# Kernel tuning notes

Hardware: AMD Instinct MI355X
Metric: run time of the kernel (lower is better)

The kernel has to match this reference:

```python
import jax, jax.numpy as jnp
import numpy as np

B = 65536


def conv1d(x, w, b=None, stride=1, pad=0):
    # x: [B, C_in, L], w: [C_out, C_in, K]
    y = jax.lax.conv_general_dilated(x, w, (stride,), [(pad, pad)],
                                     dimension_numbers=('NCH', 'OIH', 'NCH'))
    if b is not None:
        y = y + b[None, :, None]
    return y


def setup_inputs() -> dict:
    key = jax.random.key(0)
    ks = jax.random.split(key, 17)
    s = 0.05
    return {
        'data': jax.random.normal(ks[0], (B, 512), jnp.float32),
        'sr': 16000,
        'stft_w': jax.random.normal(ks[1], (258, 1, 256), jnp.float32) * s,
        'e1_w': jax.random.normal(ks[2], (128, 129, 3), jnp.float32) * s,
        'e1_b': jax.random.normal(ks[3], (128,), jnp.float32) * s,
        'e2_w': jax.random.normal(ks[4], (64, 128, 3), jnp.float32) * s,
        'e2_b': jax.random.normal(ks[5], (64,), jnp.float32) * s,
        'e3_w': jax.random.normal(ks[6], (64, 64, 3), jnp.float32) * s,
        'e3_b': jax.random.normal(ks[7], (64,), jnp.float32) * s,
        'e4_w': jax.random.normal(ks[8], (128, 64, 3), jnp.float32) * s,
        'e4_b': jax.random.normal(ks[9], (128,), jnp.float32) * s,
        'w_ih': jax.random.normal(ks[10], (512, 128), jnp.float32) * s,
        'w_hh': jax.random.normal(ks[11], (512, 128), jnp.float32) * s,
        'b_ih': jax.random.normal(ks[12], (512,), jnp.float32) * s,
        'b_hh': jax.random.normal(ks[13], (512,), jnp.float32) * s,
        'dec_w': jax.random.normal(ks[14], (1, 128, 1), jnp.float32) * s,
        'dec_b': jax.random.normal(ks[15], (1,), jnp.float32) * s,
    }


def reference(data, sr, stft_w, e1_w, e1_b, e2_w, e2_b, e3_w, e3_b,
              e4_w, e4_b, w_ih, w_hh, b_ih, b_hh, dec_w, dec_b):
    # First streaming call: zero context, zero LSTM state.
    context_size = 64 if sr == 16000 else 32
    b = data.shape[0]
    ctx = jnp.zeros((b, context_size), data.dtype)
    x = jnp.concatenate([ctx, data], axis=1)          # [B, 576]
    # --- STFT: reflect-pad right by 64, strided conv ---
    x = jnp.pad(x, ((0, 0), (0, 64)), mode='reflect')[:, None, :]  # [B,1,640]
    spec = conv1d(x, stft_w, None, stride=128)         # [B,258,4]
    real = spec[:, :129, :6]
    imag = spec[:, 129:, :6]
    mag = jnp.sqrt(real * real + imag * imag)          # [B,129,4]
    # --- encoder: 4 conv1d + relu blocks ---
    x = jax.nn.relu(conv1d(mag, e1_w, e1_b, 1, 1))     # [B,128,4]
    x = jax.nn.relu(conv1d(x, e2_w, e2_b, 2, 1))       # [B,64,2]
    x = jax.nn.relu(conv1d(x, e3_w, e3_b, 2, 1))       # [B,64,1]
    x = jax.nn.relu(conv1d(x, e4_w, e4_b, 1, 1))       # [B,128,1]
    # --- decoder: LSTMCell (zero initial state) ---
    xt = x[:, :, 0]                                    # squeeze(-1): [B,128]
    h0 = jnp.zeros((b, 128), xt.dtype)
    c0 = jnp.zeros((b, 128), xt.dtype)
    gates = xt @ w_ih.T + b_ih + h0 @ w_hh.T + b_hh    # [B,512]
    i, f, g, o = jnp.split(gates, 4, axis=1)           # torch gate order i,f,g,o
    c = jax.nn.sigmoid(f) * c0 + jax.nn.sigmoid(i) * jnp.tanh(g)
    h = jax.nn.sigmoid(o) * jnp.tanh(c)
    # Dropout is identity in eval mode; then relu, 1x1 conv, sigmoid.
    y = jax.nn.relu(h)[:, :, None]                     # [B,128,1]
    y = jax.nn.sigmoid(conv1d(y, dec_w, dec_b, 1, 0))  # [B,1,1]
    return y
```

## Files before the change

### kernel.cpp

```cpp
#include <hip/hip_runtime.h>


typedef unsigned short u16;
typedef unsigned int u32;
typedef __attribute__((ext_vector_type(8))) short bf16x8;
typedef __attribute__((ext_vector_type(4))) float f32x4;

__device__ __forceinline__ float bf2f(u16 u) {
    return __uint_as_float(((u32)u) << 16);
}
__device__ __forceinline__ u16 f2bf(float f) {
    u32 x = __float_as_uint(f);
    return (u16)((x + 0x7fffu + ((x >> 16) & 1u)) >> 16);
}
__device__ __forceinline__ float sigm(float x) {
    return 1.0f / (1.0f + __expf(-x));
}
__device__ __forceinline__ float tanh_f(float x) {
    float e = __expf(2.0f * x);
    return 1.0f - 2.0f / (e + 1.0f);
}
__device__ __forceinline__ float ldany(const void* p, int idx, int fp32) {
    if (fp32) return ((const float*)p)[idx];
    return bf2f(((const u16*)p)[idx]);
}
__device__ __forceinline__ bf16x8 as_h(uint4 v) {
    union { uint4 u; bf16x8 h; } x; x.u = v; return x.h;
}
#define MFMA(A_, B_, C_) __builtin_amdgcn_mfma_f32_16x16x32_bf16((A_), (B_), (C_), 0, 0, 0)

#define O_WST  0
#define O_W1   34816
#define O_W2   61440
#define O_W3   74752
#define O_W4   78848
#define O_WIH  82944
#define O_B1   115712
#define O_B2   115840
#define O_B3   115904
#define O_B4   115968
#define O_BIH  116096
#define O_DECW 116608
#define O_DECB 116736
#define O_FLAG 116737
#define NCVT   116737

__global__ __launch_bounds__(256) void vad_detect(const void* __restrict__ stft,
                                                  float* __restrict__ dst) {
    if (threadIdx.x == 0 && blockIdx.x == 0) {
        const u16* p = (const u16*)stft;
        int huge = 0;
        for (int i = 0; i < 32; i++) {
            float v = bf2f(p[i]);
            if (!(v == v) || fabsf(v) > 1.0e4f) huge = 1;
        }
        dst[O_FLAG] = huge ? 1.0f : 0.0f;
    }
}

__global__ __launch_bounds__(256) void SileroVAD_83829171683562_kernel(
    void* __restrict__ out, int n, const float* __restrict__ flagp) {
    int i = blockIdx.x * 256 + threadIdx.x;
    int fp32 = (flagp[O_FLAG] != 0.0f);
    if (i < n) {
        if (fp32) ((float*)out)[i] = 0.25f;
        else      ((u16*)out)[i]   = 0x3E80;
    }
}

__device__ __forceinline__ u16 wq_stft(const void* s, int fp32, int j, int k) {
    if (j >= 258) return 0;
    int o = (j >> 1) + (j & 1) * 129;
    return f2bf(ldany(s, o * 256 + k, fp32));
}
__device__ __forceinline__ u16 wq_e1(const void* s, int fp32, int j, int k) {
    if (k >= 408) return 0;
    int tap = k / 136, f = k - tap * 136;
    if (f >= 129) return 0;
    return f2bf(ldany(s, (j * 129 + f) * 3 + tap, fp32));
}
__device__ __forceinline__ u16 wq_e2(const void* s, int fp32, int j, int k) {
    if (k >= 408) return 0;
    int tap = k / 136, c = k - tap * 136;
    if (c >= 128) return 0;
    return f2bf(ldany(s, (j * 128 + c) * 3 + tap, fp32));
}

__global__ __launch_bounds__(256) void vad_cvt_w(
    const void* __restrict__ stft, const void* __restrict__ e1w,
    const void* __restrict__ e1b,  const void* __restrict__ e2w,
    const void* __restrict__ e2b,  const void* __restrict__ e3w,
    const void* __restrict__ e3b,  const void* __restrict__ e4w,
    const void* __restrict__ e4b,  const void* __restrict__ wih,
    const void* __restrict__ bih,  const void* __restrict__ bhh,
    const void* __restrict__ decw, const void* __restrict__ decb,
    float* __restrict__ dst)
{
    int i = blockIdx.x * 256 + threadIdx.x;
    if (i >= NCVT) return;
    int fp32 = (dst[O_FLAG] != 0.0f);
    u32* D = (u32*)dst;
    if (i < O_W1) {
        int t = i * 2, j = t >> 8, k = t & 255;
        D[i] = (u32)wq_stft(stft, fp32, j, k) | ((u32)wq_stft(stft, fp32, j, k + 1) << 16);
    } else if (i < O_W2) {
        int t = (i - O_W1) * 2, j = t / 416, k = t - j * 416;
        D[i] = (u32)wq_e1(e1w, fp32, j, k) | ((u32)wq_e1(e1w, fp32, j, k + 1) << 16);
    } else if (i < O_W3) {
        int t = (i - O_W2) * 2, j = t / 416, k = t - j * 416;
        D[i] = (u32)wq_e2(e2w, fp32, j, k) | ((u32)wq_e2(e2w, fp32, j, k + 1) << 16);
    } else if (i < O_W4) {
        int t = (i - O_W3) * 2, j = t >> 7, c0 = (t & 127) >> 1;
        u16 lo = f2bf(ldany(e3w, (j * 64 + c0) * 3 + 1, fp32));
        u16 hi = f2bf(ldany(e3w, (j * 64 + c0) * 3 + 2, fp32));
        D[i] = (u32)lo | ((u32)hi << 16);
    } else if (i < O_WIH) {
        int t = (i - O_W4) * 2, j = t >> 6, k = t & 63;
        u16 lo = f2bf(ldany(e4w, (j * 64 + k) * 3 + 1, fp32));
        u16 hi = f2bf(ldany(e4w, (j * 64 + k + 1) * 3 + 1, fp32));
        D[i] = (u32)lo | ((u32)hi << 16);
    } else if (i < O_B1) {
        int t = (i - O_WIH) * 2;
        u16 lo = f2bf(ldany(wih, t, fp32));
        u16 hi = f2bf(ldany(wih, t + 1, fp32));
        D[i] = (u32)lo | ((u32)hi << 16);
    } else if (i < O_B2)  dst[i] = ldany(e1b, i - O_B1, fp32);
    else if (i < O_B3)    dst[i] = ldany(e2b, i - O_B2, fp32);
    else if (i < O_B4)    dst[i] = ldany(e3b, i - O_B3, fp32);
    else if (i < O_BIH)   dst[i] = ldany(e4b, i - O_B4, fp32);
    else if (i < O_DECW) { int j = i - O_BIH; dst[i] = ldany(bih, j, fp32) + ldany(bhh, j, fp32); }
    else if (i < O_DECB)  dst[i] = ldany(decw, i - O_DECW, fp32);
    else                  dst[i] = ldany(decb, 0, fp32);
}

__device__ __forceinline__ uint4 load_x8(const void* data, int fp32, int e, int p0) {
    uint4 v;
    if (p0 < 64) { v.x = v.y = v.z = v.w = 0u; return v; }
    if (p0 < 576) {
        if (!fp32)
            return *(const uint4*)((const u16*)data + (size_t)e * 512u + (unsigned)(p0 - 64));
        const float* s = (const float*)data + (size_t)e * 512u + (unsigned)(p0 - 64);
        v.x = (u32)f2bf(s[0]) | ((u32)f2bf(s[1]) << 16);
        v.y = (u32)f2bf(s[2]) | ((u32)f2bf(s[3]) << 16);
        v.z = (u32)f2bf(s[4]) | ((u32)f2bf(s[5]) << 16);
        v.w = (u32)f2bf(s[6]) | ((u32)f2bf(s[7]) << 16);
        return v;
    }
    u16 t[8];
    #pragma unroll
    for (int b = 0; b < 8; b++) {
        int d = 1086 - (p0 + b);
        t[b] = fp32 ? f2bf(((const float*)data)[(size_t)e * 512u + d])
                    : ((const u16*)data)[(size_t)e * 512u + d];
    }
    v.x = (u32)t[0] | ((u32)t[1] << 16);
    v.y = (u32)t[2] | ((u32)t[3] << 16);
    v.z = (u32)t[4] | ((u32)t[5] << 16);
    v.w = (u32)t[6] | ((u32)t[7] << 16);
    return v;
}

#define EB 16
__global__ __launch_bounds__(512, 6) void vad_fused(const void* __restrict__ data,
                                                    const float* __restrict__ W,
                                                    void* __restrict__ out)
{
    __shared__ __align__(16) char smem[48400];
    u16*   XH    = (u16*)smem;
    u16*   OUT1  = (u16*)smem;
    u16*   MAGE1 = (u16*)(smem + 22272);
    u16*   OUT2  = (u16*)(smem + 22272);
    u16*   OUT3  = (u16*)(smem + 30592);
    u16*   OUT4  = (u16*)(smem + 32896);
    float* REDU  = (float*)(smem + 37248);

    const int tid  = threadIdx.x;
    const int w    = __builtin_amdgcn_readfirstlane(tid >> 6);
    const int l    = tid & 63;
    const int l15  = l & 15;
    const int lg   = l >> 4;
    const int b0   = blockIdx.x * EB;
    const int fp32 = (W[O_FLAG] != 0.0f);

    for (int tau = tid; tau < 1280; tau += 512) {
        int ridx = tau >> 4, c8 = tau & 15;
        int e = ridx / 5, h = ridx - e * 5;
        uint4 v = load_x8(data, fp32, b0 + e, h * 128 + c8 * 8);
        *(uint4*)(XH + e * 680 + h * 136 + c8 * 8) = v;
    }
    for (int i = tid; i < 2176; i += 512) {
        int e = i / 136, k = i - e * 136;
        int off = (k < 68) ? k : (k - 68 + 340);
        ((u32*)(MAGE1 + e * 816))[off] = 0u;
    }
    for (int i = tid; i < 448; i += 512) {
        int e = i / 28, r = i - e * 28;
        MAGE1[e * 816 + (r / 7 + 1) * 136 + 129 + (r % 7)] = 0;
    }
    if (tid < 8) MAGE1[16 * 816 + tid] = 0;
    __syncthreads();

    {
        const u16* WB = (const u16*)(W + O_WST);
        const u16* xb0 = XH + (l15 >> 2) * 680 + (l15 & 3) * 136 + lg * 8;
        #pragma unroll 1
        for (int q = 0; q < 3; q++) {
            if (q == 2 && w != 7) break;
            int nt = (q < 2) ? (w * 2 + q) : 16;
            const u16* bp = WB + (nt * 16 + l15) * 256 + lg * 8;
            f32x4 a0 = {0.f,0.f,0.f,0.f}, a1 = {0.f,0.f,0.f,0.f};
            f32x4 a2 = {0.f,0.f,0.f,0.f}, a3 = {0.f,0.f,0.f,0.f};
            uint4 b_0 = *(const uint4*)(bp);
            uint4 b_1 = *(const uint4*)(bp + 32);
            uint4 b_2 = *(const uint4*)(bp + 64);
            uint4 b_3 = *(const uint4*)(bp + 96);
            #pragma unroll 1
            for (int kk = 0; kk < 8; kk++) {
                int kn = (kk < 4) ? (kk + 4) : 7;
                uint4 bn = *(const uint4*)(bp + kn * 32);
                int ao = (kk >> 2) * 136 + (kk & 3) * 32;
                bf16x8 bh = as_h(b_0);
                a0 = MFMA(as_h(*(const uint4*)(xb0 + ao)),        bh, a0);
                a1 = MFMA(as_h(*(const uint4*)(xb0 + 2720 + ao)), bh, a1);
                a2 = MFMA(as_h(*(const uint4*)(xb0 + 5440 + ao)), bh, a2);
                a3 = MFMA(as_h(*(const uint4*)(xb0 + 8160 + ao)), bh, a3);
                b_0 = b_1; b_1 = b_2; b_2 = b_3; b_3 = bn;
            }
            int f = nt * 8 + (l15 >> 1);
            bool wr = ((l15 & 1) == 0) && (f <= 128);
#define ST1_EPI(MT, ACC) do { \
            _Pragma("unroll") \
            for (int r = 0; r < 4; r++) { \
                float v_ = ACC[r]; \
                float p_ = __shfl_xor(v_, 1); \
                float m_ = sqrtf(v_ * v_ + p_ * p_); \
                if (wr) MAGE1[((MT) * 4 + lg) * 816 + (r + 1) * 136 + f] = f2bf(m_); \
            } \
        } while (0)
            ST1_EPI(0, a0); ST1_EPI(1, a1); ST1_EPI(2, a2); ST1_EPI(3, a3);
        }
    }
    __syncthreads();

    for (int i = tid; i < 1472; i += 512) {
        int e = i / 92, k = i - e * 92;
        u32* bz = (u32*)(OUT1 + e * 696);
        int off;
        if (k < 68)      off = k;
        else if (k < 84) { int z = k - 68; off = (z / 4 + 1) * 68 + 64 + (z & 3); }
        else             off = 340 + (k - 84);
        bz[off] = 0u;
    }

    {
        const u16* WB = (const u16*)(W + O_W1);
        const u16* ar0 = MAGE1 + (l15 >> 2) * 816 + (l15 & 3) * 136 + lg * 8;
        int j = w * 16 + l15;
        const u16* bp = WB + j * 416 + lg * 8;
        float bias = W[O_B1 + j];
        f32x4 a0 = {0.f,0.f,0.f,0.f}, a1 = {0.f,0.f,0.f,0.f};
        f32x4 a2 = {0.f,0.f,0.f,0.f}, a3 = {0.f,0.f,0.f,0.f};
        uint4 b_0 = *(const uint4*)(bp);
        uint4 b_1 = *(const uint4*)(bp + 32);
        uint4 b_2 = *(const uint4*)(bp + 64);
        uint4 b_3 = *(const uint4*)(bp + 96);
        #pragma unroll 1
        for (int kk = 0; kk < 13; kk++) {
            int kn = (kk < 9) ? (kk + 4) : 12;
            uint4 bn = *(const uint4*)(bp + kn * 32);
            int ao = kk * 32;
            bf16x8 bh = as_h(b_0);
            a0 = MFMA(as_h(*(const uint4*)(ar0 + ao)),        bh, a0);
            a1 = MFMA(as_h(*(const uint4*)(ar0 + 3264 + ao)), bh, a1);
            a2 = MFMA(as_h(*(const uint4*)(ar0 + 6528 + ao)), bh, a2);
            a3 = MFMA(as_h(*(const uint4*)(ar0 + 9792 + ao)), bh, a3);
            b_0 = b_1; b_1 = b_2; b_2 = b_3; b_3 = bn;
        }
#define ST2_EPI(MT, ACC) do { \
        _Pragma("unroll") \
        for (int r = 0; r < 4; r++) { \
            float v_ = ACC[r] + bias; \
            OUT1[((MT) * 4 + lg) * 696 + (r + 1) * 136 + j] = f2bf(v_ > 0.f ? v_ : 0.f); \
        } \
    } while (0)
        ST2_EPI(0, a0); ST2_EPI(1, a1); ST2_EPI(2, a2); ST2_EPI(3, a3);
    }
    __syncthreads();

    {
        const u16* WB = (const u16*)(W + O_W2);
        int jt = w >> 1, mh = w & 1;
        int j = jt * 16 + l15;
        const u16* bp = WB + j * 416 + lg * 8;
        float bias = W[O_B2 + j];
        const u16* ar0 = OUT1 + (l15 >> 1) * 696 + (l15 & 1) * 272 + lg * 8
                              + mh * 5568;
        f32x4 a0 = {0.f,0.f,0.f,0.f};
        uint4 b_0 = *(const uint4*)(bp);
        uint4 b_1 = *(const uint4*)(bp + 32);
        uint4 b_2 = *(const uint4*)(bp + 64);
        uint4 b_3 = *(const uint4*)(bp + 96);
        #pragma unroll 1
        for (int kk = 0; kk < 13; kk++) {
            int kn = (kk < 9) ? (kk + 4) : 12;
            uint4 bn = *(const uint4*)(bp + kn * 32);
            bf16x8 bh = as_h(b_0);
            a0 = MFMA(as_h(*(const uint4*)(ar0 + kk * 32)), bh, a0);
            b_0 = b_1; b_1 = b_2; b_2 = b_3; b_3 = bn;
        }
        #pragma unroll
        for (int r = 0; r < 4; r++) {
            int rg = mh * 16 + lg * 4 + r;
            float v_ = a0[r] + bias;
            OUT2[(rg >> 1) * 260 + 2 * j + (rg & 1)] = f2bf(v_ > 0.f ? v_ : 0.f);
        }
    }
    __syncthreads();

    if (w < 4) {
        const u16* ap = OUT2 + l15 * 260 + lg * 8;
        const u16* WB = (const u16*)(W + O_W3);
        int j = w * 16 + l15;
        const u16* bp = WB + j * 128 + lg * 8;
        f32x4 acc = {0.f, 0.f, 0.f, 0.f};
        #pragma unroll 1
        for (int kk = 0; kk < 4; kk++)
            acc = MFMA(as_h(*(const uint4*)(ap + kk * 32)),
                       as_h(*(const uint4*)(bp + kk * 32)), acc);
        float bias = W[O_B3 + j];
        #pragma unroll
        for (int r = 0; r < 4; r++) {
            float v = acc[r] + bias;
            OUT3[(lg * 4 + r) * 72 + j] = f2bf(v > 0.f ? v : 0.f);
        }
    }
    __syncthreads();

    {
        const u16* ap = OUT3 + l15 * 72 + lg * 8;
        uint4 a0 = *(const uint4*)(ap);
        uint4 a1 = *(const uint4*)(ap + 32);
        const u16* WB = (const u16*)(W + O_W4);
        int j = w * 16 + l15;
        const u16* bp = WB + j * 64 + lg * 8;
        f32x4 acc = {0.f, 0.f, 0.f, 0.f};
        acc = MFMA(as_h(a0), as_h(*(const uint4*)(bp)), acc);
        acc = MFMA(as_h(a1), as_h(*(const uint4*)(bp + 32)), acc);
        float bias = W[O_B4 + j];
        #pragma unroll
        for (int r = 0; r < 4; r++) {
            float v = acc[r] + bias;
            OUT4[(lg * 4 + r) * 136 + j] = f2bf(v > 0.f ? v : 0.f);
        }
    }
    __syncthreads();

    {
        const u16* ap = OUT4 + l15 * 136 + lg * 8;
        const u16* WB = (const u16*)(W + O_WIH);
        int c = w * 16 + l15;
        const u16* bi = WB + c * 128 + lg * 8;
        f32x4 gi = {0.f,0.f,0.f,0.f}, gg = {0.f,0.f,0.f,0.f}, go = {0.f,0.f,0.f,0.f};
        uint4 Bi = *(const uint4*)(bi);
        uint4 Bg = *(const uint4*)(bi + 32768);
        uint4 Bo = *(const uint4*)(bi + 49152);
        #pragma unroll 1
        for (int kk = 0; kk < 4; kk++) {
            int kn = (kk < 3) ? (kk + 1) : 3;
            uint4 Ni = *(const uint4*)(bi + kn * 32);
            uint4 Ng = *(const uint4*)(bi + 32768 + kn * 32);
            uint4 No = *(const uint4*)(bi + 49152 + kn * 32);
            bf16x8 av = as_h(*(const uint4*)(ap + kk * 32));
            gi = MFMA(av, as_h(Bi), gi);
            gg = MFMA(av, as_h(Bg), gg);
            go = MFMA(av, as_h(Bo), go);
            Bi = Ni; Bg = Ng; Bo = No;
        }
        float bI = W[O_BIH + c], bG = W[O_BIH + 256 + c], bO = W[O_BIH + 384 + c];
        float dw = W[O_DECW + c];
        float part[4];
        #pragma unroll
        for (int r = 0; r < 4; r++) {
            float cs = sigm(gi[r] + bI) * tanh_f(gg[r] + bG);
            float h  = sigm(go[r] + bO) * tanh_f(cs);
            h = h > 0.f ? h : 0.f;
            part[r] = dw * h;
        }
        #pragma unroll
        for (int mk = 1; mk < 16; mk <<= 1) {
            #pragma unroll
            for (int r = 0; r < 4; r++) part[r] += __shfl_xor(part[r], mk);
        }
        if (l15 == 0) {
            #pragma unroll
            for (int r = 0; r < 4; r++) REDU[w * 16 + lg * 4 + r] = part[r];
        }
    }
    __syncthreads();

    if (tid < 16) {
        float s = 0.f;
        #pragma unroll
        for (int ww = 0; ww < 8; ww++) s += REDU[ww * 16 + tid];
        float y = sigm(s + W[O_DECB]);
        if (fp32) ((float*)out)[b0 + tid] = y;
        else      ((u16*)out)[b0 + tid]   = f2bf(y);
    }
}

extern "C" void kernel_launch(void* const* d_in, const int* in_sizes, int n_in,
                              void* d_out, int out_size, void* d_ws, size_t ws_size,
                              hipStream_t stream) {
    (void)in_sizes; (void)n_in; (void)ws_size;
    float* Wf = (float*)d_ws;

    vad_detect<<<1, 64, 0, stream>>>(d_in[2], Wf);

    SileroVAD_83829171683562_kernel<<<(out_size + 255) / 256, 256, 0, stream>>>(
        d_out, out_size, Wf);

    vad_cvt_w<<<(NCVT + 255) / 256, 256, 0, stream>>>(
        d_in[2],  d_in[3],  d_in[4],  d_in[5],  d_in[6],  d_in[7],
        d_in[8],  d_in[9],  d_in[10], d_in[11], d_in[13], d_in[14],
        d_in[15], d_in[16], Wf);

    vad_fused<<<65536 / EB, 512, 0, stream>>>(d_in[0], Wf, d_out);
}
```

Baseline: 448.8 us.

## Fold dtype detection into weight conversion and tighten MFMA loop epilogues

Removes the standalone dtype-detect kernel by having every block of the weight-conversion kernel recompute the flag with a wave vote, saving one launch. In the fused kernel it shortens the B-operand prefetch depth from 4 to 2 and unrolls the MFMA loops. It also swaps sqrtf for raw v_sqrt_f32 and per-element rounding for packed v_cvt_pk_bf16_f32 in the epilogues. The shallower prefetch lowers register pressure but may expose more global-load latency, and the fast sqrt differs slightly in precision.

```diff
diff --git a/kernel.cpp b/kernel.cpp
--- a/kernel.cpp
+++ b/kernel.cpp
@@ -12,6 +12,13 @@
 __device__ __forceinline__ u16 f2bf(float f) {
     u32 x = __float_as_uint(f);
     return (u16)((x + 0x7fffu + ((x >> 16) & 1u)) >> 16);
+}
+__device__ __forceinline__ float sqrt_fast(float x) {
+    float r; asm("v_sqrt_f32 %0, %1" : "=v"(r) : "v"(x)); return r;
+}
+__device__ __forceinline__ u32 cvtpk_bf16(float lo, float hi) {
+    u32 r; asm("v_cvt_pk_bf16_f32 %0, %1, %2" : "=v"(r) : "v"(lo), "v"(hi));
+    return r;
 }
 __device__ __forceinline__ float sigm(float x) {
     return 1.0f / (1.0f + __expf(-x));
@@ -45,19 +52,6 @@
 #define O_FLAG 116737
 #define NCVT   116737
 
-__global__ __launch_bounds__(256) void vad_detect(const void* __restrict__ stft,
-                                                  float* __restrict__ dst) {
-    if (threadIdx.x == 0 && blockIdx.x == 0) {
-        const u16* p = (const u16*)stft;
-        int huge = 0;
-        for (int i = 0; i < 32; i++) {
-            float v = bf2f(p[i]);
-            if (!(v == v) || fabsf(v) > 1.0e4f) huge = 1;
-        }
-        dst[O_FLAG] = huge ? 1.0f : 0.0f;
-    }
-}
-
 __global__ __launch_bounds__(256) void SileroVAD_83829171683562_kernel(
     void* __restrict__ out, int n, const float* __restrict__ flagp) {
     int i = blockIdx.x * 256 + threadIdx.x;
@@ -96,9 +90,23 @@
     const void* __restrict__ decw, const void* __restrict__ decb,
     float* __restrict__ dst)
 {
+    __shared__ int sflag;
+    {
+        int huge = 0;
+        if (threadIdx.x < 64) {
+            if (threadIdx.x < 32) {
+                float v = bf2f(((const u16*)stft)[threadIdx.x]);
+                if (!(v == v) || fabsf(v) > 1.0e4f) huge = 1;
+            }
+            huge = __any(huge);
+            if (threadIdx.x == 0) sflag = huge;
+        }
+        __syncthreads();
+    }
+    int fp32 = sflag;
     int i = blockIdx.x * 256 + threadIdx.x;
+    if (blockIdx.x == 0 && threadIdx.x == 0) dst[O_FLAG] = fp32 ? 1.0f : 0.0f;
     if (i >= NCVT) return;
-    int fp32 = (dst[O_FLAG] != 0.0f);
     u32* D = (u32*)dst;
     if (i < O_W1) {
         int t = i * 2, j = t >> 8, k = t & 255;
@@ -212,11 +220,9 @@
             f32x4 a2 = {0.f,0.f,0.f,0.f}, a3 = {0.f,0.f,0.f,0.f};
             uint4 b_0 = *(const uint4*)(bp);
             uint4 b_1 = *(const uint4*)(bp + 32);
-            uint4 b_2 = *(const uint4*)(bp + 64);
-            uint4 b_3 = *(const uint4*)(bp + 96);
-            #pragma unroll 1
+            #pragma unroll 4
             for (int kk = 0; kk < 8; kk++) {
-                int kn = (kk < 4) ? (kk + 4) : 7;
+                int kn = (kk < 6) ? (kk + 2) : 7;
                 uint4 bn = *(const uint4*)(bp + kn * 32);
                 int ao = (kk >> 2) * 136 + (kk & 3) * 32;
                 bf16x8 bh = as_h(b_0);
@@ -224,17 +230,24 @@
                 a1 = MFMA(as_h(*(const uint4*)(xb0 + 2720 + ao)), bh, a1);
                 a2 = MFMA(as_h(*(const uint4*)(xb0 + 5440 + ao)), bh, a2);
                 a3 = MFMA(as_h(*(const uint4*)(xb0 + 8160 + ao)), bh, a3);
-                b_0 = b_1; b_1 = b_2; b_2 = b_3; b_3 = bn;
+                b_0 = b_1; b_1 = bn;
             }
             int f = nt * 8 + (l15 >> 1);
             bool wr = ((l15 & 1) == 0) && (f <= 128);
 #define ST1_EPI(MT, ACC) do { \
+            float m_[4]; \
             _Pragma("unroll") \
             for (int r = 0; r < 4; r++) { \
                 float v_ = ACC[r]; \
                 float p_ = __shfl_xor(v_, 1); \
-                float m_ = sqrtf(v_ * v_ + p_ * p_); \
-                if (wr) MAGE1[((MT) * 4 + lg) * 816 + (r + 1) * 136 + f] = f2bf(m_); \
+                m_[r] = sqrt_fast(v_ * v_ + p_ * p_); \
+            } \
+            u32 pkA_ = cvtpk_bf16(m_[0], m_[1]); \
+            u32 pkB_ = cvtpk_bf16(m_[2], m_[3]); \
+            if (wr) { \
+                u16* mb_ = MAGE1 + ((MT) * 4 + lg) * 816 + f; \
+                mb_[136] = (u16)pkA_; mb_[272] = (u16)(pkA_ >> 16); \
+                mb_[408] = (u16)pkB_; mb_[544] = (u16)(pkB_ >> 16); \
             } \
         } while (0)
             ST1_EPI(0, a0); ST1_EPI(1, a1); ST1_EPI(2, a2); ST1_EPI(3, a3);
@@ -262,11 +275,9 @@
         f32x4 a2 = {0.f,0.f,0.f,0.f}, a3 = {0.f,0.f,0.f,0.f};
         uint4 b_0 = *(const uint4*)(bp);
         uint4 b_1 = *(const uint4*)(bp + 32);
-        uint4 b_2 = *(const uint4*)(bp + 64);
-        uint4 b_3 = *(const uint4*)(bp + 96);
-        #pragma unroll 1
+        #pragma unroll 4
         for (int kk = 0; kk < 13; kk++) {
-            int kn = (kk < 9) ? (kk + 4) : 12;
+            int kn = (kk < 11) ? (kk + 2) : 12;
             uint4 bn = *(const uint4*)(bp + kn * 32);
             int ao = kk * 32;
             bf16x8 bh = as_h(b_0);
@@ -274,14 +285,18 @@
             a1 = MFMA(as_h(*(const uint4*)(ar0 + 3264 + ao)), bh, a1);
             a2 = MFMA(as_h(*(const uint4*)(ar0 + 6528 + ao)), bh, a2);
             a3 = MFMA(as_h(*(const uint4*)(ar0 + 9792 + ao)), bh, a3);
-            b_0 = b_1; b_1 = b_2; b_2 = b_3; b_3 = bn;
+            b_0 = b_1; b_1 = bn;
         }
 #define ST2_EPI(MT, ACC) do { \
-        _Pragma("unroll") \
-        for (int r = 0; r < 4; r++) { \
-            float v_ = ACC[r] + bias; \
-            OUT1[((MT) * 4 + lg) * 696 + (r + 1) * 136 + j] = f2bf(v_ > 0.f ? v_ : 0.f); \
-        } \
+        float r0_ = fmaxf(ACC[0] + bias, 0.f); \
+        float r1_ = fmaxf(ACC[1] + bias, 0.f); \
+        float r2_ = fmaxf(ACC[2] + bias, 0.f); \
+        float r3_ = fmaxf(ACC[3] + bias, 0.f); \
+        u32 pA_ = cvtpk_bf16(r0_, r1_); \
+        u32 pB_ = cvtpk_bf16(r2_, r3_); \
+        u16* ob_ = OUT1 + ((MT) * 4 + lg) * 696 + j; \
+        ob_[136] = (u16)pA_; ob_[272] = (u16)(pA_ >> 16); \
+        ob_[408] = (u16)pB_; ob_[544] = (u16)(pB_ >> 16); \
     } while (0)
         ST2_EPI(0, a0); ST2_EPI(1, a1); ST2_EPI(2, a2); ST2_EPI(3, a3);
     }
@@ -298,22 +313,20 @@
         f32x4 a0 = {0.f,0.f,0.f,0.f};
         uint4 b_0 = *(const uint4*)(bp);
         uint4 b_1 = *(const uint4*)(bp + 32);
-        uint4 b_2 = *(const uint4*)(bp + 64);
-        uint4 b_3 = *(const uint4*)(bp + 96);
-        #pragma unroll 1
+        #pragma unroll 4
         for (int kk = 0; kk < 13; kk++) {
-            int kn = (kk < 9) ? (kk + 4) : 12;
+            int kn = (kk < 11) ? (kk + 2) : 12;
             uint4 bn = *(const uint4*)(bp + kn * 32);
             bf16x8 bh = as_h(b_0);
             a0 = MFMA(as_h(*(const uint4*)(ar0 + kk * 32)), bh, a0);
-            b_0 = b_1; b_1 = b_2; b_2 = b_3; b_3 = bn;
-        }
-        #pragma unroll
-        for (int r = 0; r < 4; r++) {
-            int rg = mh * 16 + lg * 4 + r;
-            float v_ = a0[r] + bias;
-            OUT2[(rg >> 1) * 260 + 2 * j + (rg & 1)] = f2bf(v_ > 0.f ? v_ : 0.f);
-        }
+            b_0 = b_1; b_1 = bn;
+        }
+        float r0 = fmaxf(a0[0] + bias, 0.f), r1 = fmaxf(a0[1] + bias, 0.f);
+        float r2 = fmaxf(a0[2] + bias, 0.f), r3 = fmaxf(a0[3] + bias, 0.f);
+        u32 pA = cvtpk_bf16(r0, r1), pB = cvtpk_bf16(r2, r3);
+        int qrow = mh * 8 + lg * 2;
+        *(u32*)(OUT2 + qrow * 260 + 2 * j)       = pA;
+        *(u32*)(OUT2 + (qrow + 1) * 260 + 2 * j) = pB;
     }
     __syncthreads();
 
@@ -323,35 +336,37 @@
         int j = w * 16 + l15;
         const u16* bp = WB + j * 128 + lg * 8;
         f32x4 acc = {0.f, 0.f, 0.f, 0.f};
-        #pragma unroll 1
+        #pragma unroll 2
         for (int kk = 0; kk < 4; kk++)
             acc = MFMA(as_h(*(const uint4*)(ap + kk * 32)),
                        as_h(*(const uint4*)(bp + kk * 32)), acc);
         float bias = W[O_B3 + j];
-        #pragma unroll
-        for (int r = 0; r < 4; r++) {
-            float v = acc[r] + bias;
-            OUT3[(lg * 4 + r) * 72 + j] = f2bf(v > 0.f ? v : 0.f);
-        }
+        float r0 = fmaxf(acc[0] + bias, 0.f), r1 = fmaxf(acc[1] + bias, 0.f);
+        float r2 = fmaxf(acc[2] + bias, 0.f), r3 = fmaxf(acc[3] + bias, 0.f);
+        u32 pA = cvtpk_bf16(r0, r1), pB = cvtpk_bf16(r2, r3);
+        u16* ob = OUT3 + (lg * 4) * 72 + j;
+        ob[0]   = (u16)pA; ob[72]  = (u16)(pA >> 16);
+        ob[144] = (u16)pB; ob[216] = (u16)(pB >> 16);
     }
     __syncthreads();
 
     {
         const u16* ap = OUT3 + l15 * 72 + lg * 8;
-        uint4 a0 = *(const uint4*)(ap);
-        uint4 a1 = *(const uint4*)(ap + 32);
+        uint4 a0v = *(const uint4*)(ap);
+        uint4 a1v = *(const uint4*)(ap + 32);
         const u16* WB = (const u16*)(W + O_W4);
         int j = w * 16 + l15;
         const u16* bp = WB + j * 64 + lg * 8;
         f32x4 acc = {0.f, 0.f, 0.f, 0.f};
-        acc = MFMA(as_h(a0), as_h(*(const uint4*)(bp)), acc);
-        acc = MFMA(as_h(a1), as_h(*(const uint4*)(bp + 32)), acc);
+        acc = MFMA(as_h(a0v), as_h(*(const uint4*)(bp)), acc);
+        acc = MFMA(as_h(a1v), as_h(*(const uint4*)(bp + 32)), acc);
         float bias = W[O_B4 + j];
-        #pragma unroll
-        for (int r = 0; r < 4; r++) {
-            float v = acc[r] + bias;
-            OUT4[(lg * 4 + r) * 136 + j] = f2bf(v > 0.f ? v : 0.f);
-        }
+        float r0 = fmaxf(acc[0] + bias, 0.f), r1 = fmaxf(acc[1] + bias, 0.f);
+        float r2 = fmaxf(acc[2] + bias, 0.f), r3 = fmaxf(acc[3] + bias, 0.f);
+        u32 pA = cvtpk_bf16(r0, r1), pB = cvtpk_bf16(r2, r3);
+        u16* ob = OUT4 + (lg * 4) * 136 + j;
+        ob[0]   = (u16)pA; ob[136] = (u16)(pA >> 16);
+        ob[272] = (u16)pB; ob[408] = (u16)(pB >> 16);
     }
     __syncthreads();
 
@@ -361,20 +376,12 @@
         int c = w * 16 + l15;
         const u16* bi = WB + c * 128 + lg * 8;
         f32x4 gi = {0.f,0.f,0.f,0.f}, gg = {0.f,0.f,0.f,0.f}, go = {0.f,0.f,0.f,0.f};
-        uint4 Bi = *(const uint4*)(bi);
-        uint4 Bg = *(const uint4*)(bi + 32768);
-        uint4 Bo = *(const uint4*)(bi + 49152);
-        #pragma unroll 1
+        #pragma unroll 2
         for (int kk = 0; kk < 4; kk++) {
-            int kn = (kk < 3) ? (kk + 1) : 3;
-            uint4 Ni = *(const uint4*)(bi + kn * 32);
-            uint4 Ng = *(const uint4*)(bi + 32768 + kn * 32);
-            uint4 No = *(const uint4*)(bi + 49152 + kn * 32);
             bf16x8 av = as_h(*(const uint4*)(ap + kk * 32));
-            gi = MFMA(av, as_h(Bi), gi);
-            gg = MFMA(av, as_h(Bg), gg);
-            go = MFMA(av, as_h(Bo), go);
-            Bi = Ni; Bg = Ng; Bo = No;
+            gi = MFMA(av, as_h(*(const uint4*)(bi + kk * 32)), gi);
+            gg = MFMA(av, as_h(*(const uint4*)(bi + 32768 + kk * 32)), gg);
+            go = MFMA(av, as_h(*(const uint4*)(bi + 49152 + kk * 32)), go);
         }
         float bI = W[O_BIH + c], bG = W[O_BIH + 256 + c], bO = W[O_BIH + 384 + c];
         float dw = W[O_DECW + c];
@@ -414,15 +421,13 @@
     (void)in_sizes; (void)n_in; (void)ws_size;
     float* Wf = (float*)d_ws;
 
-    vad_detect<<<1, 64, 0, stream>>>(d_in[2], Wf);
-
-    SileroVAD_83829171683562_kernel<<<(out_size + 255) / 256, 256, 0, stream>>>(
-        d_out, out_size, Wf);
-
     vad_cvt_w<<<(NCVT + 255) / 256, 256, 0, stream>>>(
         d_in[2],  d_in[3],  d_in[4],  d_in[5],  d_in[6],  d_in[7],
         d_in[8],  d_in[9],  d_in[10], d_in[11], d_in[13], d_in[14],
         d_in[15], d_in[16], Wf);
 
+    SileroVAD_83829171683562_kernel<<<(out_size + 255) / 256, 256, 0, stream>>>(
+        d_out, out_size, Wf);
+
     vad_fused<<<65536 / EB, 512, 0, stream>>>(d_in[0], Wf, d_out);
 }
```

Measured after the change: 422.6 us. 5.8% less time.
